# Kernel tuning notes

Measured on AMD Instinct MI355X. Metric: run time of the kernel, lower is better.

## Reference

```python
import jax, jax.numpy as jnp
import numpy as np

B, T, I, L, D, O = 256, 512, 512, 128, 4, 2
LN_EPS = 1e-5

def setup_inputs() -> dict:
    key = jax.random.key(0)
    ks = jax.random.split(key, 7)
    x = jax.random.normal(ks[0], (B, T, I), jnp.float32)
    # Xavier-ish scaling keeps the recurrence numerically tame
    W_in = jax.random.normal(ks[1], (L, D, I), jnp.float32) * (1.0 / np.sqrt(I))
    W_liquid = jax.random.normal(ks[2], (L, D, L), jnp.float32) * (1.0 / np.sqrt(L))
    W_gate = jax.random.normal(ks[3], (L, D), jnp.float32)
    b_liquid = jnp.zeros((L,), jnp.float32)
    W_out = jax.random.normal(ks[4], (O, L), jnp.float32) * (1.0 / np.sqrt(L))
    b_out = jnp.zeros((O,), jnp.float32)
    ln_w = jnp.ones((L,), jnp.float32)
    ln_b = jnp.zeros((L,), jnp.float32)
    leaky_rate = jnp.asarray(0.3, jnp.float32)
    return {"x": x, "W_in": W_in, "W_liquid": W_liquid, "W_gate": W_gate,
            "b_liquid": b_liquid, "W_out": W_out, "b_out": b_out,
            "ln_w": ln_w, "ln_b": ln_b, "leaky_rate": leaky_rate}

def reference(x, W_in, W_liquid, W_gate, b_liquid, W_out, b_out, ln_w, ln_b, leaky_rate):
    # Liquid dendritic RNN. Dropout is identity (eval mode).
    gate = jax.nn.sigmoid(W_gate)                                   # [L,D]
    # Input branch has no recurrent dependency -> batch it over all timesteps
    in_br = jax.nn.relu(jnp.einsum('ldi,bti->btld', W_in, x))       # [B,T,L,D]
    merged_in = jnp.einsum('btld,ld->btl', in_br, gate)             # [B,T,L]
    alpha = jax.nn.sigmoid(leaky_rate)

    def step(state, m_in_t):                                        # state [B,L]
        rec_br = jax.nn.relu(jnp.einsum('ldh,bh->bld', W_liquid, state))
        merged_rec = jnp.einsum('bld,ld->bl', rec_br, gate)
        li = m_in_t + merged_rec + b_liquid                         # [B,L]
        mu = jnp.mean(li, axis=-1, keepdims=True)
        var = jnp.var(li, axis=-1, keepdims=True)
        li = (li - mu) * jax.lax.rsqrt(var + LN_EPS) * ln_w + ln_b
        new_state = (1.0 - alpha) * state + alpha * jnp.tanh(li)
        return new_state, None

    state0 = jnp.zeros((x.shape[0], W_in.shape[0]), x.dtype)
    final_state, _ = jax.lax.scan(step, state0, jnp.swapaxes(merged_in, 0, 1))
    return final_state @ W_out.T + b_out                            # [B,O]
```

## Files before the change

kernel.cpp:

```cpp
#include <hip/hip_runtime.h>
#include <hip/hip_bf16.h>
#include <stdint.h>


typedef __bf16 bf16x8 __attribute__((ext_vector_type(8)));
typedef float f32x4_t __attribute__((ext_vector_type(4)));

__device__ inline unsigned short f2bf(float f) {
    union { float f; unsigned u; } v; v.f = f;
    unsigned r = v.u + 0x7fffu + ((v.u >> 16) & 1u);
    return (unsigned short)(r >> 16);
}

__device__ inline void lds_barrier() {
    asm volatile("s_waitcnt lgkmcnt(0)" ::: "memory");
    __builtin_amdgcn_s_barrier();
}

__device__ inline float bfly16_add(float x) {
    float a, b;
    asm volatile("v_mov_b32 %0, %2\n\t"
                 "v_mov_b32 %1, %2\n\t"
                 "v_permlane16_swap_b32 %0, %1"
                 : "=&v"(a), "=&v"(b) : "v"(x));
    return a + b;
}
__device__ inline float bfly32_add(float x) {
    float a, b;
    asm volatile("v_mov_b32 %0, %2\n\t"
                 "v_mov_b32 %1, %2\n\t"
                 "v_permlane32_swap_b32 %0, %1"
                 : "=&v"(a), "=&v"(b) : "v"(x));
    return a + b;
}

__global__ __launch_bounds__(256, 2)
void gemm_in_kernel(const float* __restrict__ x, const float* __restrict__ W_in,
                    const float* __restrict__ W_gate, const float* __restrict__ b_liq,
                    float* __restrict__ mt)
{
    __shared__ unsigned short As[128 * 32];
    __shared__ unsigned short Bs[128 * 32];

    const int tid = threadIdx.x;
    const int m0 = blockIdx.y * 128;
    const int n0 = blockIdx.x * 128;
    const int lane = tid & 63;
    const int wid  = tid >> 6;
    const int wr = wid >> 1, wc = wid & 1;
    const int fr = lane & 15, fq = lane >> 4;

    f32x4_t acc[4][4];
    #pragma unroll
    for (int i = 0; i < 4; ++i)
        #pragma unroll
        for (int j = 0; j < 4; ++j)
            acc[i][j] = (f32x4_t){0.f, 0.f, 0.f, 0.f};

    for (int k0 = 0; k0 < 512; k0 += 32) {
        #pragma unroll
        for (int p = 0; p < 4; ++p) {
            int ch = tid + p * 256;
            int r  = ch >> 3;
            int c  = ch & 7;
            float4 va = *(const float4*)(x    + (size_t)(m0 + r) * 512 + k0 + c * 4);
            float4 vb = *(const float4*)(W_in + (size_t)(n0 + r) * 512 + k0 + c * 4);
            ushort4 ha, hb;
            ha.x = f2bf(va.x); ha.y = f2bf(va.y); ha.z = f2bf(va.z); ha.w = f2bf(va.w);
            hb.x = f2bf(vb.x); hb.y = f2bf(vb.y); hb.z = f2bf(vb.z); hb.w = f2bf(vb.w);
            *(ushort4*)(&As[r * 32 + c * 4]) = ha;
            *(ushort4*)(&Bs[r * 32 + c * 4]) = hb;
        }
        __syncthreads();

        bf16x8 af[4], bfr[4];
        #pragma unroll
        for (int mi = 0; mi < 4; ++mi)
            af[mi] = *(const bf16x8*)(&As[(wr * 64 + mi * 16 + fr) * 32 + fq * 8]);
        #pragma unroll
        for (int ni = 0; ni < 4; ++ni)
            bfr[ni] = *(const bf16x8*)(&Bs[(wc * 64 + ni * 16 + fr) * 32 + fq * 8]);

        #pragma unroll
        for (int mi = 0; mi < 4; ++mi)
            #pragma unroll
            for (int ni = 0; ni < 4; ++ni)
                acc[mi][ni] = __builtin_amdgcn_mfma_f32_16x16x32_bf16(
                                  af[mi], bfr[ni], acc[mi][ni], 0, 0, 0);
        __syncthreads();
    }

    float gv[4], blq[4];
    #pragma unroll
    for (int ni = 0; ni < 4; ++ni) {
        int n = n0 + wc * 64 + ni * 16 + fr;
        gv[ni]  = 1.f / (1.f + __expf(-W_gate[n]));
        blq[ni] = b_liq[n >> 2];
    }
    #pragma unroll
    for (int mi = 0; mi < 4; ++mi) {
        #pragma unroll
        for (int ni = 0; ni < 4; ++ni) {
            int n = n0 + wc * 64 + ni * 16 + fr;
            int l = n >> 2;
            #pragma unroll
            for (int j = 0; j < 4; ++j) {
                float v = acc[mi][ni][j];
                float r = fmaxf(v, 0.f) * gv[ni];
                r += __shfl_xor(r, 1);
                r += __shfl_xor(r, 2);
                if ((lane & 3) == 0) {
                    int row = m0 + wr * 64 + mi * 16 + fq * 4 + j;
                    int bb = row >> 9;
                    int tt = row & 511;
                    mt[(size_t)bb * 65536 + (size_t)l * 512 + tt] = r + blq[ni];
                }
            }
        }
    }
}

__global__ __launch_bounds__(256, 1)
void scan_kernel(const float* __restrict__ mt, const float* __restrict__ W_liq,
                 const float* __restrict__ W_gate, const float* __restrict__ W_out,
                 const float* __restrict__ b_out, const float* __restrict__ ln_w,
                 const float* __restrict__ ln_b, const float* __restrict__ leaky,
                 float* __restrict__ out)
{
    __shared__ __align__(16) unsigned short s_bf[128];
    __shared__ __align__(16) float red2[8];
    __shared__ float s_final[128];

    const int tid  = threadIdx.x;
    const int b    = blockIdx.x;
    const int lane = tid & 63;
    const int w    = tid >> 6;
    const int fr   = lane & 15;
    const int fq   = lane >> 4;

    bf16x8 wfrag[8][4];
    #pragma unroll
    for (int mi = 0; mi < 8; ++mi) {
        const int n = w * 128 + mi * 16 + fr;
        const float gn = 1.f / (1.f + __expf(-W_gate[n]));
        const float* wrow = W_liq + (size_t)n * 128;
        #pragma unroll
        for (int kk = 0; kk < 4; ++kk) {
            float4 f0 = *(const float4*)(wrow + kk * 32 + fq * 8);
            float4 f1 = *(const float4*)(wrow + kk * 32 + fq * 8 + 4);
            union { unsigned short u[8]; bf16x8 v; } cv;
            cv.u[0] = f2bf(gn * f0.x); cv.u[1] = f2bf(gn * f0.y);
            cv.u[2] = f2bf(gn * f0.z); cv.u[3] = f2bf(gn * f0.w);
            cv.u[4] = f2bf(gn * f1.x); cv.u[5] = f2bf(gn * f1.y);
            cv.u[6] = f2bf(gn * f1.z); cv.u[7] = f2bf(gn * f1.w);
            wfrag[mi][kk] = cv.v;
        }
    }

    size_t midx[8];
    #pragma unroll
    for (int mi = 0; mi < 8; ++mi)
        midx[mi] = (size_t)b * 65536 + (size_t)(w * 32 + mi * 4 + fq) * 512;

    const int l_own  = w * 32 + (fr & 7) * 4 + fq;
    const float K2   = 2.8853900817779268f;
    const float lw2  = ln_w[l_own] * K2;
    const float lb2  = ln_b[l_own] * K2;
    const float alpha = 1.f / (1.f + __expf(-leaky[0]));
    const float oma   = 1.f - alpha;
    const float n2a   = -2.f * alpha;

    float s_own = 0.f;
    float c0    = alpha;

    float4 cur4[8], nxt4[8];
    #pragma unroll
    for (int mi = 0; mi < 8; ++mi) cur4[mi] = *(const float4*)(mt + midx[mi]);
    #pragma unroll
    for (int mi = 0; mi < 8; ++mi) nxt4[mi] = *(const float4*)(mt + midx[mi] + 4);

    if (tid < 64) ((unsigned*)s_bf)[tid] = 0u;
    lds_barrier();

    const f32x4_t z = {0.f, 0.f, 0.f, 0.f};

    for (int ts = 0; ts < 512; ts += 4) {
        float4 ld4[8];
        if (ts < 504) {
            #pragma unroll
            for (int mi = 0; mi < 8; ++mi)
                ld4[mi] = *(const float4*)(mt + midx[mi] + ts + 8);
        }

        #pragma unroll
        for (int ph = 0; ph < 4; ++ph) {
            bf16x8 bfr[4];
            #pragma unroll
            for (int kk = 0; kk < 4; ++kk)
                bfr[kk] = *(const bf16x8*)(&s_bf[kk * 32 + fq * 8]);

            f32x4_t a0[8], a1[8];
            #pragma unroll
            for (int mi = 0; mi < 8; ++mi) {
                a0[mi] = __builtin_amdgcn_mfma_f32_16x16x32_bf16(wfrag[mi][0], bfr[0], z, 0, 0, 0);
                a1[mi] = __builtin_amdgcn_mfma_f32_16x16x32_bf16(wfrag[mi][2], bfr[2], z, 0, 0, 0);
            }
            #pragma unroll
            for (int mi = 0; mi < 8; ++mi) {
                a0[mi] = __builtin_amdgcn_mfma_f32_16x16x32_bf16(wfrag[mi][1], bfr[1], a0[mi], 0, 0, 0);
                a1[mi] = __builtin_amdgcn_mfma_f32_16x16x32_bf16(wfrag[mi][3], bfr[3], a1[mi], 0, 0, 0);
            }

            float li[8];
            float v1a = 0.f, v1b = 0.f, v2a = 0.f, v2b = 0.f;
            #pragma unroll
            for (int mi = 0; mi < 8; ++mi) {
                f32x4_t s4 = a0[mi] + a1[mi];
                float mr = (fmaxf(s4[0], 0.f) + fmaxf(s4[1], 0.f))
                         + (fmaxf(s4[2], 0.f) + fmaxf(s4[3], 0.f));
                li[mi] = cur4[mi][ph] + mr;
                if (mi & 1) { v1b += li[mi]; v2b = fmaf(li[mi], li[mi], v2b); }
                else        { v1a += li[mi]; v2a = fmaf(li[mi], li[mi], v2a); }
            }
            float v1 = v1a + v1b, v2 = v2a + v2b;

            float sa = (fr & 1) ? li[1] : li[0];
            float sb = (fr & 1) ? li[3] : li[2];
            float sc = (fr & 1) ? li[5] : li[4];
            float sd = (fr & 1) ? li[7] : li[6];
            float se = (fr & 2) ? sb : sa;
            float sf = (fr & 2) ? sd : sc;
            float li_o = (fr & 4) ? sf : se;

            v1 = bfly16_add(v1);  v2 = bfly16_add(v2);
            v1 = bfly32_add(v1);  v2 = bfly32_add(v2);
            if (lane == 0) { red2[2 * w] = v1; red2[2 * w + 1] = v2; }
            lds_barrier();

            float4 r0 = *(const float4*)&red2[0], r1 = *(const float4*)&red2[4];
            float S1 = (r0.x + r0.z) + (r1.x + r1.z);
            float S2 = (r0.y + r0.w) + (r1.y + r1.w);
            float mean = S1 * (1.f / 128.f);
            float var  = fmaf(-mean, mean, S2 * (1.f / 128.f));
            float rstd = __builtin_amdgcn_rsqf(var + 1e-5f);

            float q  = rstd * lw2;
            float xn = fmaf(li_o, q, fmaf(-mean, q, lb2));
            float e  = __builtin_amdgcn_exp2f(xn);
            float r  = __builtin_amdgcn_rcpf(e + 1.f);
            s_own    = fmaf(n2a, r, c0);
            c0       = fmaf(oma, s_own, alpha);

            unsigned cvt;
            asm("v_cvt_pk_bf16_f32 %0, %1, %2" : "=v"(cvt) : "v"(s_own), "v"(0.f));
            if (fr < 8) s_bf[l_own] = (unsigned short)cvt;
            lds_barrier();
        }

        #pragma unroll
        for (int mi = 0; mi < 8; ++mi) cur4[mi] = nxt4[mi];
        if (ts < 504) {
            #pragma unroll
            for (int mi = 0; mi < 8; ++mi) nxt4[mi] = ld4[mi];
        }
    }

    if (fr < 8) s_final[l_own] = s_own;
    __syncthreads();
    if (tid < 2) {
        float accO = b_out[tid];
        #pragma unroll
        for (int h = 0; h < 128; ++h)
            accO = fmaf(s_final[h], W_out[tid * 128 + h], accO);
        out[b * 2 + tid] = accO;
    }
}

extern "C" void kernel_launch(void* const* d_in, const int* in_sizes, int n_in,
                              void* d_out, int out_size, void* d_ws, size_t ws_size,
                              hipStream_t stream)
{
    const float* x      = (const float*)d_in[0];
    const float* W_in   = (const float*)d_in[1];
    const float* W_liq  = (const float*)d_in[2];
    const float* W_gate = (const float*)d_in[3];
    const float* b_liq  = (const float*)d_in[4];
    const float* W_out  = (const float*)d_in[5];
    const float* b_out  = (const float*)d_in[6];
    const float* ln_w   = (const float*)d_in[7];
    const float* ln_b   = (const float*)d_in[8];
    const float* leaky  = (const float*)d_in[9];
    float* out = (float*)d_out;
    float* mt  = (float*)d_ws;

    gemm_in_kernel<<<dim3(4, 1024), 256, 0, stream>>>(x, W_in, W_gate, b_liq, mt);
    scan_kernel<<<256, 256, 0, stream>>>(mt, W_liq, W_gate,
                                         W_out, b_out, ln_w, ln_b, leaky, out);
}
```

Baseline: 646.9 us.

## Replace second per-step barrier with redundant state update and ds_bpermute broadcast

Each wave now stores its pre-normalisation values into a double-buffered LDS array next to the reduction partials, so one barrier per timestep suffices. Every wave then redundantly computes the full 128-element new state (two elements per lane) and builds its bf16 MFMA B-fragments through ds_bpermute lane shuffles, with no LDS write followed by a second barrier and reload. This removes one workgroup barrier per step from the serial recurrence. In exchange each wave does extra transcendental work and 16 bpermutes per step, and it relies on double buffering to avoid a write-after-read race.

```diff
diff --git a/kernel.cpp b/kernel.cpp
--- a/kernel.cpp
+++ b/kernel.cpp
@@ -127,8 +127,8 @@
                  const float* __restrict__ ln_b, const float* __restrict__ leaky,
                  float* __restrict__ out)
 {
-    __shared__ __align__(16) unsigned short s_bf[128];
-    __shared__ __align__(16) float red2[8];
+    __shared__ __align__(16) float li_buf[2][128];
+    __shared__ __align__(16) float red2[2][8];
     __shared__ float s_final[128];
 
     const int tid  = threadIdx.x;
@@ -162,25 +162,26 @@
     for (int mi = 0; mi < 8; ++mi)
         midx[mi] = (size_t)b * 65536 + (size_t)(w * 32 + mi * 4 + fq) * 512;
 
-    const int l_own  = w * 32 + (fr & 7) * 4 + fq;
-    const float K2   = 2.8853900817779268f;
-    const float lw2  = ln_w[l_own] * K2;
-    const float lb2  = ln_b[l_own] * K2;
+    const int   h0  = 2 * lane;
+    const float K2  = 2.8853900817779268f;
+    const float lw20 = ln_w[h0] * K2,     lb20 = ln_b[h0] * K2;
+    const float lw21 = ln_w[h0 + 1] * K2, lb21 = ln_b[h0 + 1] * K2;
     const float alpha = 1.f / (1.f + __expf(-leaky[0]));
     const float oma   = 1.f - alpha;
     const float n2a   = -2.f * alpha;
 
-    float s_own = 0.f;
-    float c0    = alpha;
+    float s0 = 0.f, s1 = 0.f;
+    float c00 = alpha, c01 = alpha;
+
+    bf16x8 bfr[4];
+    #pragma unroll
+    for (int kk = 0; kk < 4; ++kk) bfr[kk] = (bf16x8)(__bf16)0.0f;
 
     float4 cur4[8], nxt4[8];
     #pragma unroll
     for (int mi = 0; mi < 8; ++mi) cur4[mi] = *(const float4*)(mt + midx[mi]);
     #pragma unroll
     for (int mi = 0; mi < 8; ++mi) nxt4[mi] = *(const float4*)(mt + midx[mi] + 4);
-
-    if (tid < 64) ((unsigned*)s_bf)[tid] = 0u;
-    lds_barrier();
 
     const f32x4_t z = {0.f, 0.f, 0.f, 0.f};
 
@@ -194,10 +195,7 @@
 
         #pragma unroll
         for (int ph = 0; ph < 4; ++ph) {
-            bf16x8 bfr[4];
-            #pragma unroll
-            for (int kk = 0; kk < 4; ++kk)
-                bfr[kk] = *(const bf16x8*)(&s_bf[kk * 32 + fq * 8]);
+            const int pb = ph & 1;
 
             f32x4_t a0[8], a1[8];
             #pragma unroll
@@ -234,27 +232,46 @@
 
             v1 = bfly16_add(v1);  v2 = bfly16_add(v2);
             v1 = bfly32_add(v1);  v2 = bfly32_add(v2);
-            if (lane == 0) { red2[2 * w] = v1; red2[2 * w + 1] = v2; }
+            if (lane == 0) { red2[pb][2 * w] = v1; red2[pb][2 * w + 1] = v2; }
+            if (fr < 8) li_buf[pb][w * 32 + fr * 4 + fq] = li_o;
             lds_barrier();
 
-            float4 r0 = *(const float4*)&red2[0], r1 = *(const float4*)&red2[4];
+            float4 r0 = *(const float4*)&red2[pb][0], r1 = *(const float4*)&red2[pb][4];
             float S1 = (r0.x + r0.z) + (r1.x + r1.z);
             float S2 = (r0.y + r0.w) + (r1.y + r1.w);
             float mean = S1 * (1.f / 128.f);
             float var  = fmaf(-mean, mean, S2 * (1.f / 128.f));
             float rstd = __builtin_amdgcn_rsqf(var + 1e-5f);
 
-            float q  = rstd * lw2;
-            float xn = fmaf(li_o, q, fmaf(-mean, q, lb2));
-            float e  = __builtin_amdgcn_exp2f(xn);
-            float r  = __builtin_amdgcn_rcpf(e + 1.f);
-            s_own    = fmaf(n2a, r, c0);
-            c0       = fmaf(oma, s_own, alpha);
-
-            unsigned cvt;
-            asm("v_cvt_pk_bf16_f32 %0, %1, %2" : "=v"(cvt) : "v"(s_own), "v"(0.f));
-            if (fr < 8) s_bf[l_own] = (unsigned short)cvt;
-            lds_barrier();
+            float2 liv = *(const float2*)&li_buf[pb][h0];
+
+            float q0  = rstd * lw20;
+            float xn0 = fmaf(liv.x, q0, fmaf(-mean, q0, lb20));
+            float e0  = __builtin_amdgcn_exp2f(xn0);
+            float t0  = __builtin_amdgcn_rcpf(e0 + 1.f);
+            s0  = fmaf(n2a, t0, c00);
+            c00 = fmaf(oma, s0, alpha);
+
+            float q1  = rstd * lw21;
+            float xn1 = fmaf(liv.y, q1, fmaf(-mean, q1, lb21));
+            float e1  = __builtin_amdgcn_exp2f(xn1);
+            float t1  = __builtin_amdgcn_rcpf(e1 + 1.f);
+            s1  = fmaf(n2a, t1, c01);
+            c01 = fmaf(oma, s1, alpha);
+
+            unsigned sreg;
+            asm("v_cvt_pk_bf16_f32 %0, %1, %2" : "=v"(sreg) : "v"(s0), "v"(s1));
+
+            #pragma unroll
+            for (int kk = 0; kk < 4; ++kk) {
+                union { int i[4]; bf16x8 v; } u;
+                #pragma unroll
+                for (int wd = 0; wd < 4; ++wd) {
+                    int srcb = (kk * 16 + fq * 4 + wd) * 4;
+                    u.i[wd] = __builtin_amdgcn_ds_bpermute(srcb, (int)sreg);
+                }
+                bfr[kk] = u.v;
+            }
         }
 
         #pragma unroll
@@ -265,7 +282,7 @@
         }
     }
 
-    if (fr < 8) s_final[l_own] = s_own;
+    if (w == 0) { s_final[h0] = s0; s_final[h0 + 1] = s1; }
     __syncthreads();
     if (tid < 2) {
         float accO = b_out[tid];
```

Result: slower. 717.1 us (+10.8%).
